# Performance work log

Hardware: AMD Instinct MI355X
Metric: run time of the kernel (lower is better)

## Reference

```python
import jax, jax.numpy as jnp
from jax import lax
import numpy as np

D_STATE = 16
DT_RANK = 16
D_INNER = 512
D_MODEL = 256


def _silu(x):
    return x * jax.nn.sigmoid(x)


def _ln(x, g, b):
    mu = jnp.mean(x, -1, keepdims=True)
    v = jnp.mean((x - mu) ** 2, -1, keepdims=True)
    return (x - mu) / jnp.sqrt(v + 1e-5) * g + b


def _mamba(x, Win, Wc, bc, Wx, Wdt, bdt, Alog, Dp, Wout):
    # x: [B, T, 256]; mamba_ssm defaults: expand=2, d_state=16, d_conv=4
    B, T, _ = x.shape
    xz = x @ Win.T                       # [B,T,1024]
    xc, z = jnp.split(xz, 2, axis=-1)    # each [B,T,512]
    # causal depthwise conv over time
    xt = jnp.transpose(xc, (0, 2, 1))    # [B,512,T]
    xt = lax.conv_general_dilated(xt, Wc[:, None, :], (1,), [(3, 0)],
                                  feature_group_count=D_INNER,
                                  dimension_numbers=('NCH', 'OIH', 'NCH'))
    xc = _silu(jnp.transpose(xt + bc[None, :, None], (0, 2, 1)))  # [B,T,512]
    dbl = xc @ Wx.T                      # [B,T,48]
    dt = jax.nn.softplus(dbl[..., :DT_RANK] @ Wdt.T + bdt)        # [B,T,512]
    Bm = dbl[..., DT_RANK:DT_RANK + D_STATE]                      # [B,T,16]
    Cm = dbl[..., DT_RANK + D_STATE:]                             # [B,T,16]
    A = -jnp.exp(Alog)                   # [512,16]
    dA = jnp.exp(dt[..., None] * A)                               # [B,T,512,16]
    dBu = dt[..., None] * Bm[:, :, None, :] * xc[..., None]       # [B,T,512,16]

    def step(h, inp):
        dA_t, dBu_t, C_t = inp
        h = dA_t * h + dBu_t
        return h, jnp.einsum('bdn,bn->bd', h, C_t)

    h0 = jnp.zeros((B, D_INNER, D_STATE), x.dtype)
    _, ys = lax.scan(step, h0, (jnp.moveaxis(dA, 1, 0),
                                jnp.moveaxis(dBu, 1, 0),
                                jnp.moveaxis(Cm, 1, 0)))
    y = jnp.moveaxis(ys, 0, 1) + xc * Dp
    y = y * _silu(z)
    return y @ Wout.T


def _forward(x1, x2, x3, x4, audio_feature,
             ln_g, ln_b, in_proj_w, conv_w, conv_b, xproj_w,
             dt_w, dt_b, A_log, D, out_proj_w, gate_w, gate_b):
    bt = x1.shape[0]
    gates = []
    for i in range(4):          # 4 independent 3-layer Mamba encoders
        a = audio_feature
        for l in range(3):      # Mamba_channel_temporal_block: a = ln(a); a = a + mamba(a)
            a = _ln(a, ln_g[i, l], ln_b[i, l])
            a = a + _mamba(a, in_proj_w[i, l], conv_w[i, l], conv_b[i, l],
                           xproj_w[i, l], dt_w[i, l], dt_b[i, l],
                           A_log[i, l], D[i, l], out_proj_w[i, l])
        gates.append(_silu(a @ gate_w[i].T + gate_b[i]))  # [B,5,256]
    g1 = gates[0].reshape(bt, 256, 1, 1)
    g2 = jnp.transpose(gates[1], (1, 0, 2)).reshape(bt, 256, 1, 1)
    g3 = jnp.transpose(gates[2], (1, 0, 2)).reshape(bt, 256, 1, 1)
    g4 = jnp.transpose(gates[3], (1, 0, 2)).reshape(bt, 256, 1, 1)
    o1 = x1 + g1 * x1   # gamma = 1
    o2 = x2 + g2 * x2
    o3 = x3 + g3 * x3
    o4 = x4 + g4 * x4
    audio_flat = audio_feature.reshape(-1, D_MODEL)[:, :, None]  # [bt,256,1]
    return (o4, o3, o2, o1, audio_flat)


def setup_inputs() -> dict:
    key = jax.random.key(0)
    ks = jax.random.split(key, 16)
    f32 = jnp.float32
    inp = {
        'x1': jax.random.normal(ks[0], (80, 256, 56, 56), f32),
        'x2': jax.random.normal(ks[1], (80, 256, 28, 28), f32),
        'x3': jax.random.normal(ks[2], (80, 256, 14, 14), f32),
        'x4': jax.random.normal(ks[3], (80, 256, 7, 7), f32),
        'audio_feature': jax.random.normal(ks[4], (16, 5, 256), f32),
        'ln_g': jnp.ones((4, 3, 256), f32),
        'ln_b': jnp.zeros((4, 3, 256), f32),
        'in_proj_w': jax.random.normal(ks[5], (4, 3, 2 * D_INNER, 256), f32) * 0.02,
        'conv_w': jax.random.normal(ks[6], (4, 3, D_INNER, 4), f32) * 0.1,
        'conv_b': jax.random.normal(ks[7], (4, 3, D_INNER), f32) * 0.02,
        'xproj_w': jax.random.normal(ks[8], (4, 3, DT_RANK + 2 * D_STATE, D_INNER), f32) * 0.02,
        'dt_w': jax.random.normal(ks[9], (4, 3, D_INNER, DT_RANK), f32) * 0.02,
        'dt_b': jax.random.normal(ks[10], (4, 3, D_INNER), f32) * 0.1 - 2.0,
        'A_log': jnp.log(jnp.tile(jnp.arange(1, D_STATE + 1, dtype=f32), (4, 3, D_INNER, 1))),
        'D': jnp.ones((4, 3, D_INNER), f32),
        'out_proj_w': jax.random.normal(ks[11], (4, 3, 256, D_INNER), f32) * 0.02,
        'gate_w': jax.random.normal(ks[12], (4, 256, 256), f32) * 0.05,
        'gate_b': jnp.zeros((4, 256), f32),
    }
    return inp


def reference(x1, x2, x3, x4, audio_feature,
              ln_g, ln_b, in_proj_w, conv_w, conv_b, xproj_w,
              dt_w, dt_b, A_log, D, out_proj_w, gate_w, gate_b):
    return _forward(x1, x2, x3, x4, audio_feature,
                    ln_g, ln_b, in_proj_w, conv_w, conv_b, xproj_w,
                    dt_w, dt_b, A_log, D, out_proj_w, gate_w, gate_b)
```

## Files before the change

kernel.cpp:

```cpp
#include <hip/hip_runtime.h>
#include <hip/hip_bf16.h>
#include <math.h>


#define NTOK 80
#define DM   256
#define DI   512

typedef float f32x4 __attribute__((ext_vector_type(4)));

__device__ __forceinline__ float silu_f(float v) {
    return v / (1.f + expf(-v));
}
__device__ __forceinline__ float dot4(float4 a, float4 b) {
    return a.x*b.x + a.y*b.y + a.z*b.z + a.w*b.w;
}

#define OFF_SG    0
#define OFF_A     81920
#define OFF_ALN   163840
#define OFF_XC    245760
#define OFF_Z     409600
#define OFF_Y     573440
#define OFF_WINR  737280
#define OFF_WOUTR 3883008
#define OFF_WXT   5455872
#define OFF_GWR   5750784

__global__ __launch_bounds__(256) void k_tr(const float* __restrict__ Win,
                                            const float* __restrict__ Wout,
                                            const float* __restrict__ Wx,
                                            const float* __restrict__ gw,
                                            float* __restrict__ ws) {
    __shared__ float4 T[4160];
    int b = blockIdx.x, tid = threadIdx.x;

    if (b < 192) {
        int il = b >> 4, s = b & 15;
        const float4* src = (const float4*)Win + (size_t)il * 65536;
        float4* dst = (float4*)(ws + OFF_WINR) + ((size_t)il * 16 + s) * 4096;
        for (int idx = tid; idx < 4096; idx += 256) {
            int jj = idx >> 6, k4 = idx & 63;
            int c = (jj < 32) ? (32 * s + jj) : (512 + 32 * s + jj - 32);
            T[jj * 65 + k4] = src[(size_t)c * 64 + k4];
        }
        __syncthreads();
        for (int idx = tid; idx < 4096; idx += 256) {
            int k4 = idx >> 6, jj = idx & 63;
            dst[idx] = T[jj * 65 + k4];
        }
    } else if (b < 288) {
        int bb = b - 192; int il = bb >> 3, s = bb & 7;
        const float4* src = (const float4*)Wout + (size_t)il * 32768;
        float4* dst = (float4*)(ws + OFF_WOUTR) + ((size_t)il * 8 + s) * 4096;
        for (int idx = tid; idx < 4096; idx += 256) {
            int jj = idx >> 7, k4 = idx & 127;
            T[jj * 129 + k4] = src[(size_t)(32 * s + jj) * 128 + k4];
        }
        __syncthreads();
        for (int idx = tid; idx < 4096; idx += 256) {
            int k4 = idx >> 5, jj = idx & 31;
            dst[idx] = T[jj * 129 + k4];
        }
    } else if (b < 312) {
        int bb = b - 288; int il = bb >> 1, h = bb & 1;
        const float4* src = (const float4*)Wx + (size_t)il * 6144;
        float4* dst = (float4*)(ws + OFF_WXT) + (size_t)il * 6144;
        for (int idx = tid; idx < 3072; idx += 256) {
            int jj = idx >> 6, k4l = idx & 63;
            T[jj * 65 + k4l] = src[(size_t)jj * 128 + 64 * h + k4l];
        }
        __syncthreads();
        for (int idx = tid; idx < 3072; idx += 256) {
            int k4l = idx / 48, jj = idx % 48;
            dst[(size_t)(64 * h + k4l) * 48 + jj] = T[jj * 65 + k4l];
        }
    } else {
        int bb = b - 312; int i = bb >> 3, s = bb & 7;
        const float4* src = (const float4*)gw + (size_t)i * 16384;
        float4* dst = (float4*)(ws + OFF_GWR) + ((size_t)i * 8 + s) * 2048;
        for (int idx = tid; idx < 2048; idx += 256) {
            int jj = idx >> 6, k4 = idx & 63;
            T[jj * 65 + k4] = src[(size_t)(32 * s + jj) * 64 + k4];
        }
        __syncthreads();
        for (int idx = tid; idx < 2048; idx += 256) {
            int k4 = idx >> 5, jj = idx & 31;
            dst[idx] = T[jj * 65 + k4];
        }
    }
}

__global__ __launch_bounds__(256) void K_in(
    const float* __restrict__ src, int srcStride,
    const float* __restrict__ ln_g, const float* __restrict__ ln_b,
    const float* __restrict__ Wc,   const float* __restrict__ bc,
    int l, float* __restrict__ ws)
{
    int blk = blockIdx.x;
    int tg = blk >> 6, i = (blk >> 4) & 3, s = blk & 15;
    int il = i * 3 + l;
    int tid = threadIdx.x, lane = tid & 63, wave = tid >> 6;
    int t0 = tg * 20;

    __shared__ __align__(16) float aln_s[20 * DM];

    const float4* s4 = (const float4*)(src + (size_t)i * srcStride);
    float4 g4 = ((const float4*)(ln_g + (size_t)il * DM))[lane];
    float4 b4 = ((const float4*)(ln_b + (size_t)il * DM))[lane];
    bool wr_aln = (s == 0);
    float4* aln_ws4 = (float4*)(ws + OFF_ALN + (size_t)i * NTOK * DM);
    for (int r = 0; r < 5; ++r) {
        int n = t0 + wave * 5 + r;
        float4 x = s4[(size_t)n * 64 + lane];
        float sm = x.x + x.y + x.z + x.w;
        #pragma unroll
        for (int o = 32; o > 0; o >>= 1) sm += __shfl_down(sm, o, 64);
        float mu = __shfl(sm, 0, 64) * (1.f / 256.f);
        float4 d = make_float4(x.x - mu, x.y - mu, x.z - mu, x.w - mu);
        float v2 = d.x*d.x + d.y*d.y + d.z*d.z + d.w*d.w;
        #pragma unroll
        for (int o = 32; o > 0; o >>= 1) v2 += __shfl_down(v2, o, 64);
        float rstd = rsqrtf(__shfl(v2, 0, 64) * (1.f / 256.f) + 1e-5f);
        float4 o4 = make_float4(d.x*rstd*g4.x + b4.x, d.y*rstd*g4.y + b4.y,
                                d.z*rstd*g4.z + b4.z, d.w*rstd*g4.w + b4.w);
        ((float4*)aln_s)[(wave * 5 + r) * 64 + lane] = o4;
        if (wr_aln) aln_ws4[(size_t)n * 64 + lane] = o4;
    }
    __syncthreads();

    int j = tid & 63, tq = tid >> 6;
    const float4* wp = (const float4*)(ws + OFF_WINR) + ((size_t)il * 16 + s) * 4096 + j;
    const float4* a4 = (const float4*)aln_s + tq * 5 * 64;
    float ac0 = 0.f, ac1 = 0.f, ac2 = 0.f, ac3 = 0.f, ac4 = 0.f;
    #pragma unroll 8
    for (int k4 = 0; k4 < 64; ++k4) {
        float4 w = wp[(size_t)k4 * 64];
        ac0 += dot4(w, a4[k4]);        ac1 += dot4(w, a4[64 + k4]);
        ac2 += dot4(w, a4[128 + k4]);  ac3 += dot4(w, a4[192 + k4]);
        ac4 += dot4(w, a4[256 + k4]);
    }
    int nb = t0 + tq * 5;
    if (j < 32) {
        int ch = 32 * s + j;
        const float* wc = Wc + ((size_t)il * DI + ch) * 4;
        float w0 = wc[0], w1 = wc[1], w2 = wc[2], w3 = wc[3];
        float bb = bc[(size_t)il * DI + ch];
        float x0 = bb + w3*ac0;
        float x1 = bb + w2*ac0 + w3*ac1;
        float x2 = bb + w1*ac0 + w2*ac1 + w3*ac2;
        float x3 = bb + w0*ac0 + w1*ac1 + w2*ac2 + w3*ac3;
        float x4 = bb + w0*ac1 + w1*ac2 + w2*ac3 + w3*ac4;
        float* xc = ws + OFF_XC + ((size_t)i * NTOK + nb) * DI + ch;
        xc[0]      = silu_f(x0);  xc[DI]     = silu_f(x1);
        xc[2*DI]   = silu_f(x2);  xc[3*DI]   = silu_f(x3);
        xc[4*DI]   = silu_f(x4);
    } else {
        int ch = 32 * s + (j - 32);
        float* z = ws + OFF_Z + ((size_t)i * NTOK + nb) * DI + ch;
        z[0] = ac0;  z[DI] = ac1;  z[2*DI] = ac2;  z[3*DI] = ac3;  z[4*DI] = ac4;
    }
}

__global__ __launch_bounds__(512) void K_scan(
    const float* __restrict__ Wdt, const float* __restrict__ bdt,
    const float* __restrict__ Alog, const float* __restrict__ Dp,
    int l, float* __restrict__ ws)
{
    int blk = blockIdx.x;
    int i = blk & 3, b = blk >> 2;
    int il = i * 3 + l;
    int tid = threadIdx.x;

    __shared__ __align__(16) float xc_l[5 * DI];
    __shared__ __align__(16) float dbl_l[240];
    __shared__ __align__(16) float xp_l[480];

    const float* xc_ws = ws + OFF_XC + ((size_t)i * NTOK + b * 5) * DI;
    for (int v = tid; v < 640; v += 512)
        ((float4*)xc_l)[v] = ((const float4*)xc_ws)[v];
    __syncthreads();

    if (tid < 480) {
        int c = tid % 48, r = (tid / 48) % 5, kh = tid / 240;
        const float4* wp = (const float4*)(ws + OFF_WXT) + (size_t)il * 6144 + c;
        const float4* x4 = (const float4*)xc_l + r * 128 + kh * 64;
        float acc = 0.f;
        #pragma unroll 8
        for (int kk = 0; kk < 64; ++kk)
            acc += dot4(wp[(size_t)(kh * 64 + kk) * 48], x4[kk]);
        xp_l[tid] = acc;
    }
    __syncthreads();
    if (tid < 240) dbl_l[tid] = xp_l[tid] + xp_l[240 + tid];
    __syncthreads();

    {
        int d = tid;
        float A[16], h[16];
        const float4* al4 = (const float4*)(Alog + ((size_t)il * DI + d) * 16);
        float4 av0 = al4[0], av1 = al4[1], av2 = al4[2], av3 = al4[3];
        A[0]=-expf(av0.x); A[1]=-expf(av0.y); A[2]=-expf(av0.z); A[3]=-expf(av0.w);
        A[4]=-expf(av1.x); A[5]=-expf(av1.y); A[6]=-expf(av1.z); A[7]=-expf(av1.w);
        A[8]=-expf(av2.x); A[9]=-expf(av2.y); A[10]=-expf(av2.z); A[11]=-expf(av2.w);
        A[12]=-expf(av3.x); A[13]=-expf(av3.y); A[14]=-expf(av3.z); A[15]=-expf(av3.w);
        #pragma unroll
        for (int n = 0; n < 16; ++n) h[n] = 0.f;
        const float4* wd4 = (const float4*)(Wdt + ((size_t)il * DI + d) * 16);
        float4 w0 = wd4[0], w1 = wd4[1], w2 = wd4[2], w3 = wd4[3];
        float bdtv = bdt[(size_t)il * DI + d];
        float dv   = Dp[(size_t)il * DI + d];
        const float* z_ws = ws + OFF_Z + ((size_t)i * NTOK + b * 5) * DI + d;
        float* y_ws       = ws + OFF_Y + ((size_t)i * NTOK + b * 5) * DI + d;
        #pragma unroll
        for (int t = 0; t < 5; ++t) {
            const float* db = dbl_l + t * 48;
            float acc = bdtv;
            acc += db[0]*w0.x + db[1]*w0.y + db[2]*w0.z + db[3]*w0.w;
            acc += db[4]*w1.x + db[5]*w1.y + db[6]*w1.z + db[7]*w1.w;
            acc += db[8]*w2.x + db[9]*w2.y + db[10]*w2.z + db[11]*w2.w;
            acc += db[12]*w3.x + db[13]*w3.y + db[14]*w3.z + db[15]*w3.w;
            float dtv = fmaxf(acc, 0.f) + log1pf(expf(-fabsf(acc)));
            float xv  = xc_l[t * DI + d];
            float zv  = z_ws[t * DI];
            float dx  = dtv * xv;
            float yacc = 0.f;
            #pragma unroll
            for (int n = 0; n < 16; ++n) {
                h[n] = expf(dtv * A[n]) * h[n] + dx * db[16 + n];
                yacc += h[n] * db[32 + n];
            }
            y_ws[t * DI] = (yacc + xv * dv) * silu_f(zv);
        }
    }
}

__global__ __launch_bounds__(256) void K_out(int l, float* __restrict__ ws)
{
    int blk = blockIdx.x;
    int tg = blk >> 5, i = (blk >> 3) & 3, s = blk & 7;
    int il = i * 3 + l;
    int tid = threadIdx.x;
    int t0 = tg * 10;

    __shared__ __align__(16) float y_l[10 * DI];
    __shared__ __align__(16) float part[2560];

    const float4* ysrc = (const float4*)(ws + OFF_Y + ((size_t)i * NTOK + t0) * DI);
    for (int v = tid; v < 1280; v += 256) ((float4*)y_l)[v] = ysrc[v];
    __syncthreads();

    {
        int j = tid & 31, kq = tid >> 5;
        const float4* wp = (const float4*)(ws + OFF_WOUTR) + ((size_t)il * 8 + s) * 4096 + j;
        const float4* yy = (const float4*)y_l;
        float acc[10];
        #pragma unroll
        for (int r = 0; r < 10; ++r) acc[r] = 0.f;
        #pragma unroll 4
        for (int kk = 0; kk < 16; ++kk) {
            int k4 = kq * 16 + kk;
            float4 w = wp[(size_t)k4 * 32];
            #pragma unroll
            for (int r = 0; r < 10; ++r) acc[r] += dot4(w, yy[r * 128 + k4]);
        }
        #pragma unroll
        for (int r = 0; r < 10; ++r) part[kq * 320 + r * 32 + j] = acc[r];
    }
    __syncthreads();
    for (int v = tid; v < 320; v += 256) {
        int r = v >> 5, j = v & 31;
        int n = t0 + r, c = 32 * s + j;
        float sum = ws[OFF_ALN + ((size_t)i * NTOK + n) * DM + c];
        #pragma unroll
        for (int kq = 0; kq < 8; ++kq) sum += part[kq * 320 + v];
        ws[OFF_A + ((size_t)i * NTOK + n) * DM + c] = sum;
    }
}

__global__ __launch_bounds__(256) void K_gates(const float* __restrict__ gb,
                                               float* __restrict__ ws)
{
    int blk = blockIdx.x;
    int tg = blk >> 5, i = (blk >> 3) & 3, s = blk & 7;
    int tid = threadIdx.x;
    int t0 = tg * 10;

    __shared__ __align__(16) float a_l[10 * DM];
    __shared__ __align__(16) float part[2560];

    const float4* asrc = (const float4*)(ws + OFF_A + ((size_t)i * NTOK + t0) * DM);
    for (int v = tid; v < 640; v += 256) ((float4*)a_l)[v] = asrc[v];
    __syncthreads();

    {
        int j = tid & 31, kq = tid >> 5;
        const float4* wp = (const float4*)(ws + OFF_GWR) + ((size_t)i * 8 + s) * 2048 + j;
        const float4* aa = (const float4*)a_l;
        float acc[10];
        #pragma unroll
        for (int r = 0; r < 10; ++r) acc[r] = 0.f;
        #pragma unroll 4
        for (int kk = 0; kk < 8; ++kk) {
            int k4 = kq * 8 + kk;
            float4 w = wp[(size_t)k4 * 32];
            #pragma unroll
            for (int r = 0; r < 10; ++r) acc[r] += dot4(w, aa[r * 64 + k4]);
        }
        #pragma unroll
        for (int r = 0; r < 10; ++r) part[kq * 320 + r * 32 + j] = acc[r];
    }
    __syncthreads();
    for (int v = tid; v < 320; v += 256) {
        int r = v >> 5, j = v & 31;
        int n = t0 + r, c = 32 * s + j;
        float acc = gb[(size_t)i * DM + c];
        #pragma unroll
        for (int kq = 0; kq < 8; ++kq) acc += part[kq * 320 + v];
        int bb = n / 5, tt = n % 5;
        int np = (i == 0) ? n : (tt * 16 + bb);
        ws[OFF_SG + ((size_t)i * NTOK + np) * DM + c] = 1.f + silu_f(acc);
    }
}

__global__ __launch_bounds__(256) void k_elem(
    const float* __restrict__ x1, const float* __restrict__ x2,
    const float* __restrict__ x3, const float* __restrict__ x4,
    const float* __restrict__ audio, const float* __restrict__ s_g,
    float* __restrict__ out) {
    int b = blockIdx.x;
    int t = threadIdx.x;

    if (b < 512) {
        const float* s = s_g + 3 * NTOK * DM;
        const f32x4* xv = (const f32x4*)x4;
        f32x4* ov = (f32x4*)out;
        const int total4 = 1003520 / 4;
        for (int v = b * 256 + t; v < total4; v += 512 * 256) {
            f32x4 x = __builtin_nontemporal_load(&xv[v]);
#pragma unroll
            for (int j = 0; j < 4; ++j) {
                int idx = v * 4 + j;
                x[j] *= s[idx / 49];
            }
            __builtin_nontemporal_store(x, &ov[v]);
        }
    } else if (b < 1024) {
        const float* s = s_g + 2 * NTOK * DM;
        const f32x4* xv = (const f32x4*)x3;
        f32x4* ov = (f32x4*)(out + 1003520);
        const int total4 = 4014080 / 4;
        for (int v = (b - 512) * 256 + t; v < total4; v += 512 * 256) {
            float f = s[v / 49];
            f32x4 x = __builtin_nontemporal_load(&xv[v]);
            x *= f;
            __builtin_nontemporal_store(x, &ov[v]);
        }
    } else if (b < 2048) {
        const float* s = s_g + 1 * NTOK * DM;
        const f32x4* xv = (const f32x4*)x2;
        f32x4* ov = (f32x4*)(out + 5017600);
        const int total4 = 16056320 / 4;
        for (int v = (b - 1024) * 256 + t; v < total4; v += 1024 * 256) {
            float f = s[v / 196];
            f32x4 x = __builtin_nontemporal_load(&xv[v]);
            x *= f;
            __builtin_nontemporal_store(x, &ov[v]);
        }
    } else if (b < 6144) {
        const float* s = s_g;
        const f32x4* xv = (const f32x4*)x1;
        f32x4* ov = (f32x4*)(out + 21073920);
        const int total4 = 64225280 / 4;
        for (int v = (b - 2048) * 256 + t; v < total4; v += 4096 * 256) {
            float f = s[v / 784];
            f32x4 x = __builtin_nontemporal_load(&xv[v]);
            x *= f;
            __builtin_nontemporal_store(x, &ov[v]);
        }
    } else {
        int idx = (b - 6144) * 256 + t;
        out[85299200 + idx] = audio[idx];
    }
}

extern "C" void kernel_launch(void* const* d_in, const int* in_sizes, int n_in,
                              void* d_out, int out_size, void* d_ws, size_t ws_size,
                              hipStream_t stream) {
    const float* x1        = (const float*)d_in[0];
    const float* x2        = (const float*)d_in[1];
    const float* x3        = (const float*)d_in[2];
    const float* x4        = (const float*)d_in[3];
    const float* audio     = (const float*)d_in[4];
    const float* ln_g      = (const float*)d_in[5];
    const float* ln_b      = (const float*)d_in[6];
    const float* in_proj_w = (const float*)d_in[7];
    const float* conv_w    = (const float*)d_in[8];
    const float* conv_b    = (const float*)d_in[9];
    const float* xproj_w   = (const float*)d_in[10];
    const float* dt_w      = (const float*)d_in[11];
    const float* dt_b      = (const float*)d_in[12];
    const float* A_log     = (const float*)d_in[13];
    const float* Dvec      = (const float*)d_in[14];
    const float* out_proj_w= (const float*)d_in[15];
    const float* gate_w    = (const float*)d_in[16];
    const float* gate_b    = (const float*)d_in[17];

    float* ws = (float*)d_ws;

    k_tr<<<344, 256, 0, stream>>>(in_proj_w, out_proj_w, xproj_w, gate_w, ws);
    for (int l = 0; l < 3; ++l) {
        const float* src = (l == 0) ? audio : (ws + OFF_A);
        int stride = (l == 0) ? 0 : NTOK * DM;
        K_in<<<256, 256, 0, stream>>>(src, stride, ln_g, ln_b, conv_w, conv_b, l, ws);
        K_scan<<<64, 512, 0, stream>>>(dt_w, dt_b, A_log, Dvec, l, ws);
        K_out<<<256, 256, 0, stream>>>(l, ws);
    }
    K_gates<<<256, 256, 0, stream>>>(gate_b, ws);
    k_elem<<<6224, 256, 0, stream>>>(x1, x2, x3, x4, audio, ws + OFF_SG,
                                     (float*)d_out);
}
```

Before: 278.2 us.

## Drop weight transpose pre-pass; read weights directly with token-per-lane GEMV kernels

Removes the pre-pass that transposed in_proj, out_proj and gate weights into workspace layouts, keeping only the small x_proj transpose. K_in, K_out and K_gates are restructured so each lane owns one token row, held in registers, and reads weight rows directly, with wave-uniform broadcast loads, splitting K across waves and reducing the partial sums in shared memory. Layer norm now uses a single-pass sum and sum-of-squares, and the causal conv reads neighbouring tokens from shared memory. The aim is to cut the transpose kernel's traffic and its launch, at the cost of heavy register use (128 floats per thread) and idle lanes beyond token 80.

```diff
diff --git a/kernel.cpp b/kernel.cpp
--- a/kernel.cpp
+++ b/kernel.cpp
@@ -22,143 +22,124 @@
 #define OFF_XC    245760
 #define OFF_Z     409600
 #define OFF_Y     573440
-#define OFF_WINR  737280
-#define OFF_WOUTR 3883008
-#define OFF_WXT   5455872
-#define OFF_GWR   5750784
-
-__global__ __launch_bounds__(256) void k_tr(const float* __restrict__ Win,
-                                            const float* __restrict__ Wout,
-                                            const float* __restrict__ Wx,
-                                            const float* __restrict__ gw,
-                                            float* __restrict__ ws) {
-    __shared__ float4 T[4160];
+#define OFF_WXT   737280
+
+__global__ __launch_bounds__(256) void k_trx(const float* __restrict__ Wx,
+                                             float* __restrict__ ws) {
+    __shared__ float4 T[3120];
     int b = blockIdx.x, tid = threadIdx.x;
-
-    if (b < 192) {
-        int il = b >> 4, s = b & 15;
-        const float4* src = (const float4*)Win + (size_t)il * 65536;
-        float4* dst = (float4*)(ws + OFF_WINR) + ((size_t)il * 16 + s) * 4096;
-        for (int idx = tid; idx < 4096; idx += 256) {
-            int jj = idx >> 6, k4 = idx & 63;
-            int c = (jj < 32) ? (32 * s + jj) : (512 + 32 * s + jj - 32);
-            T[jj * 65 + k4] = src[(size_t)c * 64 + k4];
-        }
-        __syncthreads();
-        for (int idx = tid; idx < 4096; idx += 256) {
-            int k4 = idx >> 6, jj = idx & 63;
-            dst[idx] = T[jj * 65 + k4];
-        }
-    } else if (b < 288) {
-        int bb = b - 192; int il = bb >> 3, s = bb & 7;
-        const float4* src = (const float4*)Wout + (size_t)il * 32768;
-        float4* dst = (float4*)(ws + OFF_WOUTR) + ((size_t)il * 8 + s) * 4096;
-        for (int idx = tid; idx < 4096; idx += 256) {
-            int jj = idx >> 7, k4 = idx & 127;
-            T[jj * 129 + k4] = src[(size_t)(32 * s + jj) * 128 + k4];
-        }
-        __syncthreads();
-        for (int idx = tid; idx < 4096; idx += 256) {
-            int k4 = idx >> 5, jj = idx & 31;
-            dst[idx] = T[jj * 129 + k4];
-        }
-    } else if (b < 312) {
-        int bb = b - 288; int il = bb >> 1, h = bb & 1;
-        const float4* src = (const float4*)Wx + (size_t)il * 6144;
-        float4* dst = (float4*)(ws + OFF_WXT) + (size_t)il * 6144;
-        for (int idx = tid; idx < 3072; idx += 256) {
-            int jj = idx >> 6, k4l = idx & 63;
-            T[jj * 65 + k4l] = src[(size_t)jj * 128 + 64 * h + k4l];
-        }
-        __syncthreads();
-        for (int idx = tid; idx < 3072; idx += 256) {
-            int k4l = idx / 48, jj = idx % 48;
-            dst[(size_t)(64 * h + k4l) * 48 + jj] = T[jj * 65 + k4l];
-        }
-    } else {
-        int bb = b - 312; int i = bb >> 3, s = bb & 7;
-        const float4* src = (const float4*)gw + (size_t)i * 16384;
-        float4* dst = (float4*)(ws + OFF_GWR) + ((size_t)i * 8 + s) * 2048;
-        for (int idx = tid; idx < 2048; idx += 256) {
-            int jj = idx >> 6, k4 = idx & 63;
-            T[jj * 65 + k4] = src[(size_t)(32 * s + jj) * 64 + k4];
-        }
-        __syncthreads();
-        for (int idx = tid; idx < 2048; idx += 256) {
-            int k4 = idx >> 5, jj = idx & 31;
-            dst[idx] = T[jj * 65 + k4];
-        }
+    int il = b >> 1, h = b & 1;
+    const float4* src = (const float4*)Wx + (size_t)il * 6144;
+    float4* dst = (float4*)(ws + OFF_WXT) + (size_t)il * 6144;
+    for (int idx = tid; idx < 3072; idx += 256) {
+        int jj = idx >> 6, k4l = idx & 63;
+        T[jj * 65 + k4l] = src[(size_t)jj * 128 + 64 * h + k4l];
+    }
+    __syncthreads();
+    for (int idx = tid; idx < 3072; idx += 256) {
+        int k4l = idx / 48, jj = idx % 48;
+        dst[(size_t)(64 * h + k4l) * 48 + jj] = T[jj * 65 + k4l];
     }
 }
 
 __global__ __launch_bounds__(256) void K_in(
     const float* __restrict__ src, int srcStride,
     const float* __restrict__ ln_g, const float* __restrict__ ln_b,
+    const float* __restrict__ Win,
     const float* __restrict__ Wc,   const float* __restrict__ bc,
     int l, float* __restrict__ ws)
 {
     int blk = blockIdx.x;
-    int tg = blk >> 6, i = (blk >> 4) & 3, s = blk & 15;
+    int i = blk >> 6, cg = blk & 63;
     int il = i * 3 + l;
-    int tid = threadIdx.x, lane = tid & 63, wave = tid >> 6;
-    int t0 = tg * 20;
-
-    __shared__ __align__(16) float aln_s[20 * DM];
-
-    const float4* s4 = (const float4*)(src + (size_t)i * srcStride);
-    float4 g4 = ((const float4*)(ln_g + (size_t)il * DM))[lane];
-    float4 b4 = ((const float4*)(ln_b + (size_t)il * DM))[lane];
-    bool wr_aln = (s == 0);
-    float4* aln_ws4 = (float4*)(ws + OFF_ALN + (size_t)i * NTOK * DM);
-    for (int r = 0; r < 5; ++r) {
-        int n = t0 + wave * 5 + r;
-        float4 x = s4[(size_t)n * 64 + lane];
-        float sm = x.x + x.y + x.z + x.w;
-        #pragma unroll
-        for (int o = 32; o > 0; o >>= 1) sm += __shfl_down(sm, o, 64);
-        float mu = __shfl(sm, 0, 64) * (1.f / 256.f);
-        float4 d = make_float4(x.x - mu, x.y - mu, x.z - mu, x.w - mu);
-        float v2 = d.x*d.x + d.y*d.y + d.z*d.z + d.w*d.w;
-        #pragma unroll
-        for (int o = 32; o > 0; o >>= 1) v2 += __shfl_down(v2, o, 64);
-        float rstd = rsqrtf(__shfl(v2, 0, 64) * (1.f / 256.f) + 1e-5f);
-        float4 o4 = make_float4(d.x*rstd*g4.x + b4.x, d.y*rstd*g4.y + b4.y,
-                                d.z*rstd*g4.z + b4.z, d.w*rstd*g4.w + b4.w);
-        ((float4*)aln_s)[(wave * 5 + r) * 64 + lane] = o4;
-        if (wr_aln) aln_ws4[(size_t)n * 64 + lane] = o4;
-    }
-    __syncthreads();
-
-    int j = tid & 63, tq = tid >> 6;
-    const float4* wp = (const float4*)(ws + OFF_WINR) + ((size_t)il * 16 + s) * 4096 + j;
-    const float4* a4 = (const float4*)aln_s + tq * 5 * 64;
-    float ac0 = 0.f, ac1 = 0.f, ac2 = 0.f, ac3 = 0.f, ac4 = 0.f;
-    #pragma unroll 8
-    for (int k4 = 0; k4 < 64; ++k4) {
-        float4 w = wp[(size_t)k4 * 64];
-        ac0 += dot4(w, a4[k4]);        ac1 += dot4(w, a4[64 + k4]);
-        ac2 += dot4(w, a4[128 + k4]);  ac3 += dot4(w, a4[192 + k4]);
-        ac4 += dot4(w, a4[256 + k4]);
-    }
-    int nb = t0 + tq * 5;
-    if (j < 32) {
-        int ch = 32 * s + j;
-        const float* wc = Wc + ((size_t)il * DI + ch) * 4;
-        float w0 = wc[0], w1 = wc[1], w2 = wc[2], w3 = wc[3];
-        float bb = bc[(size_t)il * DI + ch];
-        float x0 = bb + w3*ac0;
-        float x1 = bb + w2*ac0 + w3*ac1;
-        float x2 = bb + w1*ac0 + w2*ac1 + w3*ac2;
-        float x3 = bb + w0*ac0 + w1*ac1 + w2*ac2 + w3*ac3;
-        float x4 = bb + w0*ac1 + w1*ac2 + w2*ac3 + w3*ac4;
-        float* xc = ws + OFF_XC + ((size_t)i * NTOK + nb) * DI + ch;
-        xc[0]      = silu_f(x0);  xc[DI]     = silu_f(x1);
-        xc[2*DI]   = silu_f(x2);  xc[3*DI]   = silu_f(x3);
-        xc[4*DI]   = silu_f(x4);
+    int tid = threadIdx.x, lane = tid & 63, w = tid >> 6;
+    int th = w & 1, kh = w >> 1;
+    int n = th * 64 + lane;
+    bool act = n < NTOK;
+    int c0 = cg * 16;
+
+    __shared__ float red_s[2][NTOK][2];
+    __shared__ float comb[2][16][NTOK];
+    __shared__ float xzc[16][NTOK];
+
+    f32x4 av[32];
+    float s1 = 0.f, s2 = 0.f;
+    if (act) {
+        const f32x4* r4 = (const f32x4*)(src + (size_t)i * srcStride
+                                         + (size_t)n * DM + kh * 128);
+        #pragma unroll
+        for (int j = 0; j < 32; ++j) {
+            av[j] = r4[j];
+            s1 += av[j].x + av[j].y + av[j].z + av[j].w;
+            s2 += av[j].x*av[j].x + av[j].y*av[j].y + av[j].z*av[j].z + av[j].w*av[j].w;
+        }
+        red_s[kh][n][0] = s1;
+        red_s[kh][n][1] = s2;
+    }
+    __syncthreads();
+    if (act) {
+        float mu  = (red_s[0][n][0] + red_s[1][n][0]) * (1.f / 256.f);
+        float var = (red_s[0][n][1] + red_s[1][n][1]) * (1.f / 256.f) - mu * mu;
+        float rstd = rsqrtf(var + 1e-5f);
+        const f32x4* g4 = (const f32x4*)(ln_g + (size_t)il * DM + kh * 128);
+        const f32x4* b4 = (const f32x4*)(ln_b + (size_t)il * DM + kh * 128);
+        #pragma unroll
+        for (int j = 0; j < 32; ++j)
+            av[j] = (av[j] - mu) * rstd * g4[j] + b4[j];
+        if (cg == 0) {
+            f32x4* alnw = (f32x4*)(ws + OFF_ALN + ((size_t)i * NTOK + n) * DM + kh * 128);
+            #pragma unroll
+            for (int j = 0; j < 32; ++j) alnw[j] = av[j];
+        }
+    }
+
+    float acc[16];
+    const float* wb = Win + ((size_t)il * 1024 + c0) * DM + kh * 128;
+    #pragma unroll
+    for (int cc = 0; cc < 16; ++cc) {
+        const f32x4* w4 = (const f32x4*)(wb + cc * DM);
+        float a0 = 0.f;
+        #pragma unroll
+        for (int j = 0; j < 32; ++j) {
+            f32x4 wv = w4[j];
+            a0 += wv.x*av[j].x + wv.y*av[j].y + wv.z*av[j].z + wv.w*av[j].w;
+        }
+        acc[cc] = a0;
+    }
+    if (act) {
+        #pragma unroll
+        for (int cc = 0; cc < 16; ++cc) comb[kh][cc][n] = acc[cc];
+    }
+    __syncthreads();
+
+    if (cg >= 32) {
+        if (kh == 0 && act) {
+            int zc0 = c0 - 512;
+            #pragma unroll
+            for (int cc = 0; cc < 16; ++cc)
+                ws[OFF_Z + ((size_t)i * NTOK + n) * DI + zc0 + cc] =
+                    comb[0][cc][n] + comb[1][cc][n];
+        }
     } else {
-        int ch = 32 * s + (j - 32);
-        float* z = ws + OFF_Z + ((size_t)i * NTOK + nb) * DI + ch;
-        z[0] = ac0;  z[DI] = ac1;  z[2*DI] = ac2;  z[3*DI] = ac3;  z[4*DI] = ac4;
+        if (kh == 0 && act) {
+            #pragma unroll
+            for (int cc = 0; cc < 16; ++cc)
+                xzc[cc][n] = comb[0][cc][n] + comb[1][cc][n];
+        }
+        __syncthreads();
+        if (kh == 0 && act) {
+            int t = n % 5;
+            #pragma unroll
+            for (int cc = 0; cc < 16; ++cc) {
+                int ch = c0 + cc;
+                const float* wc = Wc + ((size_t)il * DI + ch) * 4;
+                float x = bc[(size_t)il * DI + ch] + wc[3] * xzc[cc][n];
+                if (t >= 1) x += wc[2] * xzc[cc][n - 1];
+                if (t >= 2) x += wc[1] * xzc[cc][n - 2];
+                if (t >= 3) x += wc[0] * xzc[cc][n - 3];
+                ws[OFF_XC + ((size_t)i * NTOK + n) * DI + ch] = silu_f(x);
+            }
+        }
     }
 }
 
@@ -205,7 +186,7 @@
         A[8]=-expf(av2.x); A[9]=-expf(av2.y); A[10]=-expf(av2.z); A[11]=-expf(av2.w);
         A[12]=-expf(av3.x); A[13]=-expf(av3.y); A[14]=-expf(av3.z); A[15]=-expf(av3.w);
         #pragma unroll
-        for (int n = 0; n < 16; ++n) h[n] = 0.f;
+        for (int nn = 0; nn < 16; ++nn) h[nn] = 0.f;
         const float4* wd4 = (const float4*)(Wdt + ((size_t)il * DI + d) * 16);
         float4 w0 = wd4[0], w1 = wd4[1], w2 = wd4[2], w3 = wd4[3];
         float bdtv = bdt[(size_t)il * DI + d];
@@ -226,100 +207,108 @@
             float dx  = dtv * xv;
             float yacc = 0.f;
             #pragma unroll
-            for (int n = 0; n < 16; ++n) {
-                h[n] = expf(dtv * A[n]) * h[n] + dx * db[16 + n];
-                yacc += h[n] * db[32 + n];
+            for (int nn = 0; nn < 16; ++nn) {
+                h[nn] = expf(dtv * A[nn]) * h[nn] + dx * db[16 + nn];
+                yacc += h[nn] * db[32 + nn];
             }
             y_ws[t * DI] = (yacc + xv * dv) * silu_f(zv);
         }
     }
 }
 
-__global__ __launch_bounds__(256) void K_out(int l, float* __restrict__ ws)
+__global__ __launch_bounds__(512) void K_out(
+    const float* __restrict__ Wout, int l, float* __restrict__ ws)
 {
     int blk = blockIdx.x;
-    int tg = blk >> 5, i = (blk >> 3) & 3, s = blk & 7;
+    int i = blk >> 5, cg = blk & 31;
     int il = i * 3 + l;
-    int tid = threadIdx.x;
-    int t0 = tg * 10;
-
-    __shared__ __align__(16) float y_l[10 * DI];
-    __shared__ __align__(16) float part[2560];
-
-    const float4* ysrc = (const float4*)(ws + OFF_Y + ((size_t)i * NTOK + t0) * DI);
-    for (int v = tid; v < 1280; v += 256) ((float4*)y_l)[v] = ysrc[v];
-    __syncthreads();
-
-    {
-        int j = tid & 31, kq = tid >> 5;
-        const float4* wp = (const float4*)(ws + OFF_WOUTR) + ((size_t)il * 8 + s) * 4096 + j;
-        const float4* yy = (const float4*)y_l;
-        float acc[10];
-        #pragma unroll
-        for (int r = 0; r < 10; ++r) acc[r] = 0.f;
-        #pragma unroll 4
-        for (int kk = 0; kk < 16; ++kk) {
-            int k4 = kq * 16 + kk;
-            float4 w = wp[(size_t)k4 * 32];
-            #pragma unroll
-            for (int r = 0; r < 10; ++r) acc[r] += dot4(w, yy[r * 128 + k4]);
-        }
-        #pragma unroll
-        for (int r = 0; r < 10; ++r) part[kq * 320 + r * 32 + j] = acc[r];
-    }
-    __syncthreads();
-    for (int v = tid; v < 320; v += 256) {
-        int r = v >> 5, j = v & 31;
-        int n = t0 + r, c = 32 * s + j;
-        float sum = ws[OFF_ALN + ((size_t)i * NTOK + n) * DM + c];
-        #pragma unroll
-        for (int kq = 0; kq < 8; ++kq) sum += part[kq * 320 + v];
-        ws[OFF_A + ((size_t)i * NTOK + n) * DM + c] = sum;
-    }
-}
-
-__global__ __launch_bounds__(256) void K_gates(const float* __restrict__ gb,
-                                               float* __restrict__ ws)
+    int tid = threadIdx.x, lane = tid & 63, w = tid >> 6;
+    int th = w & 1, kq = w >> 1;
+    int n = th * 64 + lane;
+    bool act = n < NTOK;
+    int c0 = cg * 8;
+
+    __shared__ float part[4][8][NTOK];
+
+    f32x4 yv[32];
+    if (act) {
+        const f32x4* y4 = (const f32x4*)(ws + OFF_Y + ((size_t)i * NTOK + n) * DI + kq * 128);
+        #pragma unroll
+        for (int j = 0; j < 32; ++j) yv[j] = y4[j];
+    }
+    float acc[8];
+    const float* wb = Wout + ((size_t)il * DM + c0) * DI + kq * 128;
+    #pragma unroll
+    for (int cc = 0; cc < 8; ++cc) {
+        const f32x4* w4 = (const f32x4*)(wb + cc * DI);
+        float a0 = 0.f;
+        #pragma unroll
+        for (int j = 0; j < 32; ++j) {
+            f32x4 wv = w4[j];
+            a0 += wv.x*yv[j].x + wv.y*yv[j].y + wv.z*yv[j].z + wv.w*yv[j].w;
+        }
+        acc[cc] = a0;
+    }
+    if (act) {
+        #pragma unroll
+        for (int cc = 0; cc < 8; ++cc) part[kq][cc][n] = acc[cc];
+    }
+    __syncthreads();
+    if (kq == 0 && act) {
+        #pragma unroll
+        for (int cc = 0; cc < 8; ++cc) {
+            size_t idx = ((size_t)i * NTOK + n) * DM + c0 + cc;
+            ws[OFF_A + idx] = ws[OFF_ALN + idx]
+                + part[0][cc][n] + part[1][cc][n] + part[2][cc][n] + part[3][cc][n];
+        }
+    }
+}
+
+__global__ __launch_bounds__(256) void K_gates(
+    const float* __restrict__ gw, const float* __restrict__ gb,
+    float* __restrict__ ws)
 {
     int blk = blockIdx.x;
-    int tg = blk >> 5, i = (blk >> 3) & 3, s = blk & 7;
-    int tid = threadIdx.x;
-    int t0 = tg * 10;
-
-    __shared__ __align__(16) float a_l[10 * DM];
-    __shared__ __align__(16) float part[2560];
-
-    const float4* asrc = (const float4*)(ws + OFF_A + ((size_t)i * NTOK + t0) * DM);
-    for (int v = tid; v < 640; v += 256) ((float4*)a_l)[v] = asrc[v];
-    __syncthreads();
-
-    {
-        int j = tid & 31, kq = tid >> 5;
-        const float4* wp = (const float4*)(ws + OFF_GWR) + ((size_t)i * 8 + s) * 2048 + j;
-        const float4* aa = (const float4*)a_l;
-        float acc[10];
-        #pragma unroll
-        for (int r = 0; r < 10; ++r) acc[r] = 0.f;
-        #pragma unroll 4
-        for (int kk = 0; kk < 8; ++kk) {
-            int k4 = kq * 8 + kk;
-            float4 w = wp[(size_t)k4 * 32];
-            #pragma unroll
-            for (int r = 0; r < 10; ++r) acc[r] += dot4(w, aa[r * 64 + k4]);
-        }
-        #pragma unroll
-        for (int r = 0; r < 10; ++r) part[kq * 320 + r * 32 + j] = acc[r];
-    }
-    __syncthreads();
-    for (int v = tid; v < 320; v += 256) {
-        int r = v >> 5, j = v & 31;
-        int n = t0 + r, c = 32 * s + j;
-        float acc = gb[(size_t)i * DM + c];
-        #pragma unroll
-        for (int kq = 0; kq < 8; ++kq) acc += part[kq * 320 + v];
-        int bb = n / 5, tt = n % 5;
-        int np = (i == 0) ? n : (tt * 16 + bb);
-        ws[OFF_SG + ((size_t)i * NTOK + np) * DM + c] = 1.f + silu_f(acc);
+    int i = blk >> 5, cg = blk & 31;
+    int tid = threadIdx.x, lane = tid & 63, w = tid >> 6;
+    int th = w & 1, kh = w >> 1;
+    int n = th * 64 + lane;
+    bool act = n < NTOK;
+    int c0 = cg * 8;
+
+    __shared__ float part[2][8][NTOK];
+
+    f32x4 avv[32];
+    if (act) {
+        const f32x4* a4 = (const f32x4*)(ws + OFF_A + ((size_t)i * NTOK + n) * DM + kh * 128);
+        #pragma unroll
+        for (int j = 0; j < 32; ++j) avv[j] = a4[j];
+    }
+    float acc[8];
+    const float* wb = gw + ((size_t)i * DM + c0) * DM + kh * 128;
+    #pragma unroll
+    for (int cc = 0; cc < 8; ++cc) {
+        const f32x4* w4 = (const f32x4*)(wb + cc * DM);
+        float a0 = 0.f;
+        #pragma unroll
+        for (int j = 0; j < 32; ++j) {
+            f32x4 wv = w4[j];
+            a0 += wv.x*avv[j].x + wv.y*avv[j].y + wv.z*avv[j].z + wv.w*avv[j].w;
+        }
+        acc[cc] = a0;
+    }
+    if (act) {
+        #pragma unroll
+        for (int cc = 0; cc < 8; ++cc) part[kh][cc][n] = acc[cc];
+    }
+    __syncthreads();
+    if (kh == 0 && act) {
+        int np = (i == 0) ? n : (n % 5) * 16 + n / 5;
+        #pragma unroll
+        for (int cc = 0; cc < 8; ++cc) {
+            float val = gb[(size_t)i * DM + c0 + cc] + part[0][cc][n] + part[1][cc][n];
+            ws[OFF_SG + ((size_t)i * NTOK + np) * DM + c0 + cc] = 1.f + silu_f(val);
+        }
     }
 }
 
@@ -408,15 +397,16 @@
 
     float* ws = (float*)d_ws;
 
-    k_tr<<<344, 256, 0, stream>>>(in_proj_w, out_proj_w, xproj_w, gate_w, ws);
+    k_trx<<<24, 256, 0, stream>>>(xproj_w, ws);
     for (int l = 0; l < 3; ++l) {
         const float* src = (l == 0) ? audio : (ws + OFF_A);
         int stride = (l == 0) ? 0 : NTOK * DM;
-        K_in<<<256, 256, 0, stream>>>(src, stride, ln_g, ln_b, conv_w, conv_b, l, ws);
+        K_in<<<256, 256, 0, stream>>>(src, stride, ln_g, ln_b, in_proj_w,
+                                      conv_w, conv_b, l, ws);
         K_scan<<<64, 512, 0, stream>>>(dt_w, dt_b, A_log, Dvec, l, ws);
-        K_out<<<256, 256, 0, stream>>>(l, ws);
-    }
-    K_gates<<<256, 256, 0, stream>>>(gate_b, ws);
+        K_out<<<128, 512, 0, stream>>>(out_proj_w, l, ws);
+    }
+    K_gates<<<128, 256, 0, stream>>>(gate_w, gate_b, ws);
     k_elem<<<6224, 256, 0, stream>>>(x1, x2, x3, x4, audio, ws + OFF_SG,
                                      (float*)d_out);
 }
```

Result: slower. 404.6 us (+45.4%).
